# Kernel optimization log

Measured on AMD Instinct MI355X. Metric: run time of the kernel, lower is better.

## Reference

```python
import jax, jax.numpy as jnp
import numpy as np

D_MODEL = 2048
NUM_HEADS = 16
HEAD_DIM = D_MODEL // NUM_HEADS
B, S = 2, 2048


def setup_inputs() -> dict:
    key = jax.random.key(0)
    ks = jax.random.split(key, 11)
    scale = 1.0 / np.sqrt(D_MODEL)
    inp = {
        "query": jax.random.normal(ks[0], (B, S, D_MODEL), dtype=jnp.float32),
        "key": jax.random.normal(ks[1], (B, S, D_MODEL), dtype=jnp.float32),
        "value": jax.random.normal(ks[2], (B, S, D_MODEL), dtype=jnp.float32),
        "Wq": jax.random.normal(ks[3], (D_MODEL, D_MODEL), dtype=jnp.float32) * scale,
        "bq": jax.random.normal(ks[4], (D_MODEL,), dtype=jnp.float32) * 0.01,
        "Wk": jax.random.normal(ks[5], (D_MODEL, D_MODEL), dtype=jnp.float32) * scale,
        "bk": jax.random.normal(ks[6], (D_MODEL,), dtype=jnp.float32) * 0.01,
        "Wv": jax.random.normal(ks[7], (D_MODEL, D_MODEL), dtype=jnp.float32) * scale,
        "bv": jax.random.normal(ks[8], (D_MODEL,), dtype=jnp.float32) * 0.01,
        "Wo": jax.random.normal(ks[9], (D_MODEL, D_MODEL), dtype=jnp.float32) * scale,
        "bo": jax.random.normal(ks[10], (D_MODEL,), dtype=jnp.float32) * 0.01,
    }
    return inp


def _shape(x, B, S):
    # [B, S, D] -> [B, H, S, hd]
    return x.reshape(B, S, NUM_HEADS, HEAD_DIM).transpose(0, 2, 1, 3)


def reference(query, key, value, Wq, bq, Wk, bk, Wv, bv, Wo, bo):
    B, Sq, D = query.shape
    Sk = key.shape[1]
    # Linear layers (torch: y = x @ W.T + b)
    Q = _shape(query @ Wq.T + bq, B, Sq)   # [B,H,Sq,hd]
    K = _shape(key @ Wk.T + bk, B, Sk)     # [B,H,Sk,hd]
    V = _shape(value @ Wv.T + bv, B, Sk)   # [B,H,Sk,hd]
    scores = jnp.einsum('bhqd,bhkd->bhqk', Q, K) / jnp.sqrt(jnp.float32(HEAD_DIM))
    # causal mask: triu(ones(Sq, Sk), diagonal=1)
    causal = jnp.triu(jnp.ones((Sq, Sk), dtype=bool), k=1)
    scores = jnp.where(causal[None, None, :, :], jnp.float32(-jnp.inf), scores)
    attn = jax.nn.softmax(scores, axis=-1)
    out = jnp.einsum('bhqk,bhkd->bhqd', attn, V)
    out = out.transpose(0, 2, 1, 3).reshape(B, Sq, D)
    return out @ Wo.T + bo
```

## Files before the change

### kernel.cpp

```cpp
#include <hip/hip_runtime.h>
#include <hip/hip_bf16.h>

typedef __attribute__((ext_vector_type(8))) short short8;
typedef __attribute__((ext_vector_type(4))) short s16x4;
typedef __attribute__((ext_vector_type(4))) float f32x4;

#define MFMA_BF16(A, B, C) __builtin_amdgcn_mfma_f32_16x16x32_bf16(A, B, C, 0, 0, 0)

__device__ __forceinline__ void gload_lds16(const __hip_bfloat16* g, __hip_bfloat16* l) {
  __builtin_amdgcn_global_load_lds(
      (const __attribute__((address_space(1))) unsigned int*)g,
      (__attribute__((address_space(3))) unsigned int*)l, 16, 0, 0);
}

__device__ __forceinline__ float finite_or(float x, float repl) {
  unsigned u;
  __builtin_memcpy(&u, &x, 4);
  return ((u & 0x7f800000u) == 0x7f800000u) ? repl : x;
}

__device__ __forceinline__ short bf16_bits(float x) {
  __hip_bfloat16 b = __float2bfloat16(x);
  short s;
  __builtin_memcpy(&s, &b, 2);
  return s;
}

__device__ __forceinline__ short8 pack8(f32x4 a, f32x4 b) {
  short8 r;
  r[0] = bf16_bits(a[0]); r[1] = bf16_bits(a[1]);
  r[2] = bf16_bits(a[2]); r[3] = bf16_bits(a[3]);
  r[4] = bf16_bits(b[0]); r[5] = bf16_bits(b[1]);
  r[6] = bf16_bits(b[2]); r[7] = bf16_bits(b[3]);
  return r;
}

__global__ __launch_bounds__(256) void cvt_kernel(
    const float* x0, const float* x1, const float* x2,
    const float* w0, const float* w1, const float* w2, const float* w3,
    __hip_bfloat16* y0, __hip_bfloat16* y1, __hip_bfloat16* y2,
    __hip_bfloat16* u0, __hip_bfloat16* u1, __hip_bfloat16* u2, __hip_bfloat16* u3)
{
  const int z = blockIdx.y;
  const float* s = z == 0 ? x0 : z == 1 ? x1 : z == 2 ? x2
                 : z == 3 ? w0 : z == 4 ? w1 : z == 5 ? w2 : w3;
  __hip_bfloat16* d = z == 0 ? y0 : z == 1 ? y1 : z == 2 ? y2
                    : z == 3 ? u0 : z == 4 ? u1 : z == 5 ? u2 : u3;
  const size_t n = (z < 3) ? (size_t)8388608 : (size_t)4194304;
  const size_t stride = (size_t)gridDim.x * 256 * 8;
  for (size_t i = ((size_t)blockIdx.x * 256 + threadIdx.x) * 8; i < n; i += stride) {
    f32x4 a = *(const f32x4*)(s + i);
    f32x4 b = *(const f32x4*)(s + i + 4);
    *(short8*)((short*)d + i) = pack8(a, b);
  }
}

#define GBUF 24576

__device__ __forceinline__ void stage_A(const __hip_bfloat16* Ab, __hip_bfloat16* bufA,
                                        int kcol, int t, int wave) {
#pragma unroll
  for (int r = 0; r < 2; ++r) {
    const int ci = r * 512 + t;
    const int row = ci >> 3, c = ci & 7;
    const int sc = c ^ (row & 7);
    gload_lds16(Ab + (size_t)row * 2048 + kcol + sc * 8, bufA + r * 4096 + wave * 512);
  }
}
__device__ __forceinline__ void stage_Br(const __hip_bfloat16* Bb, __hip_bfloat16* bufB,
                                         int kcol, int t, int wave, int r) {
  const int ci = r * 512 + t;
  const int row = ci >> 3, c = ci & 7;
  const int sc = c ^ (row & 7);
  gload_lds16(Bb + (size_t)row * 2048 + kcol + sc * 8, bufB + r * 4096 + wave * 512);
}

template <typename OutT, bool BIAS_ROW>
__device__ __forceinline__ void gemm8p_body(
    const __hip_bfloat16* __restrict__ A, const __hip_bfloat16* __restrict__ Bt,
    const float* __restrict__ bias, OutT* __restrict__ C,
    int m0, int n0, int N, float trip, __hip_bfloat16* sm)
{
  constexpr int K = 2048, NT = K / 64;
  const int t = threadIdx.x, wave = t >> 6, lane = t & 63;
  const int ll = lane & 15, lg = lane >> 4;
  const int wmB = (wave >> 2) * 64, wnB = (wave & 3) * 64;
  const __hip_bfloat16* Ab = A + (size_t)m0 * K;
  const __hip_bfloat16* Bb = Bt + (size_t)n0 * K;

  f32x4 acc[4][4] = {};

  stage_A(Ab, sm, 0, t, wave);
  stage_Br(Bb, sm + 8192, 0, t, wave, 0);
  stage_Br(Bb, sm + 8192, 0, t, wave, 1);
  stage_Br(Bb, sm + 8192, 0, t, wave, 2);
  stage_Br(Bb, sm + 8192, 0, t, wave, 3);
  stage_A(Ab, sm + GBUF, 64, t, wave);
  stage_Br(Bb, sm + GBUF + 8192, 64, t, wave, 0);
  stage_Br(Bb, sm + GBUF + 8192, 64, t, wave, 1);
  stage_Br(Bb, sm + GBUF + 8192, 64, t, wave, 2);
  stage_Br(Bb, sm + GBUF + 8192, 64, t, wave, 3);
  asm volatile("s_waitcnt vmcnt(6)" ::: "memory");
  __builtin_amdgcn_s_barrier();

  for (int i = 0; i < NT; ++i) {
    const __hip_bfloat16* bufA = sm + (i % 3) * GBUF;
    const __hip_bfloat16* bufB = bufA + 8192;
    const bool pf = (i + 2 < NT);
    __hip_bfloat16* pA = sm + ((i + 2) % 3) * GBUF;
    const int pk = (i + 2) * 64;

#pragma unroll
    for (int kk = 0; kk < 2; ++kk) {
      short8 af[4], bf[4];
#pragma unroll
      for (int f = 0; f < 4; ++f) {
        const int ar = wmB + f * 16 + ll;
        af[f] = *(const short8*)&bufA[ar * 64 + (((kk * 4 + lg) ^ (ar & 7)) << 3)];
        const int br = wnB + f * 16 + ll;
        bf[f] = *(const short8*)&bufB[br * 64 + (((kk * 4 + lg) ^ (br & 7)) << 3)];
      }
      if (pf) {
        if (kk == 0) {
          stage_A(Ab, pA, pk, t, wave);
          stage_Br(Bb, pA + 8192, pk, t, wave, 0);
        } else {
          stage_Br(Bb, pA + 8192, pk, t, wave, 1);
          stage_Br(Bb, pA + 8192, pk, t, wave, 2);
          stage_Br(Bb, pA + 8192, pk, t, wave, 3);
        }
      }
      asm volatile("s_waitcnt lgkmcnt(0)" ::: "memory");
      __builtin_amdgcn_sched_barrier(0);
      __builtin_amdgcn_s_setprio(1);
#pragma unroll
      for (int mi = 0; mi < 4; ++mi)
#pragma unroll
        for (int ni = 0; ni < 4; ++ni)
          acc[mi][ni] = MFMA_BF16(af[mi], bf[ni], acc[mi][ni]);
      __builtin_amdgcn_s_setprio(0);
      __builtin_amdgcn_sched_barrier(0);
    }

    const int rem = NT - 1 - i;
    if (rem >= 2) {
      asm volatile("s_waitcnt vmcnt(6)" ::: "memory");
      __builtin_amdgcn_s_barrier();
    } else if (rem == 1) {
      asm volatile("s_waitcnt vmcnt(0)" ::: "memory");
      __builtin_amdgcn_s_barrier();
    }
  }

#pragma unroll
  for (int mi = 0; mi < 4; ++mi)
#pragma unroll
    for (int ni = 0; ni < 4; ++ni) {
      const int col = n0 + wnB + ni * 16 + ll;
      const float bcol = BIAS_ROW ? 0.f : bias[col];
#pragma unroll
      for (int j = 0; j < 4; ++j) {
        const int row = m0 + wmB + mi * 16 + lg * 4 + j;
        const float bv = BIAS_ROW ? bias[row] : bcol;
        const float val = finite_or(acc[mi][ni][j] + bv, trip);
        if constexpr (__is_same(OutT, float))
          C[(size_t)row * N + col] = val;
        else
          C[(size_t)row * N + col] = __float2bfloat16(val);
      }
    }
}

__global__ __launch_bounds__(512) void gemm_qkvvt_kernel(
    const __hip_bfloat16* xq, const __hip_bfloat16* xk, const __hip_bfloat16* xv,
    const __hip_bfloat16* Wq, const __hip_bfloat16* Wk, const __hip_bfloat16* Wv,
    const float* bq, const float* bk, const float* bv,
    __hip_bfloat16* Q, __hip_bfloat16* K, __hip_bfloat16* Vt2)
{
  __shared__ __align__(16) __hip_bfloat16 sm[3 * GBUF];
  const int L = (int)blockIdx.x;
  if (L < 512) {
    const int z = L & 1;
    const int r = L >> 1;
    const int n0 = (r & 7) * 256;
    const int m0 = (r >> 3) * 128;
    gemm8p_body<__hip_bfloat16, false>(z ? xk : xq, z ? Wk : Wq, z ? bk : bq,
                                       z ? K : Q, m0, n0, 2048, 20000.0f, sm);
  } else {
    const int r = L - 512;
    const int n0 = (r & 15) * 256;
    const int m0 = (r >> 4) * 128;
    gemm8p_body<__hip_bfloat16, true>(Wv, xv, bv, Vt2, m0, n0, 4096, 30000.0f, sm);
  }
}

__global__ __launch_bounds__(512) void gemm_out_kernel(
    const __hip_bfloat16* A, const __hip_bfloat16* W, const float* b, float* C)
{
  __shared__ __align__(16) __hip_bfloat16 sm[3 * GBUF];
  gemm8p_body<float, false>(A, W, b, C, (int)blockIdx.y * 128,
                            (int)blockIdx.x * 256, 2048, 50000.0f, sm);
}

__global__ __launch_bounds__(256) void attn_kernel(
    const __hip_bfloat16* __restrict__ Qb, const __hip_bfloat16* __restrict__ Kb,
    const __hip_bfloat16* __restrict__ Vt, __hip_bfloat16* __restrict__ Ob)
{
  constexpr int S = 2048, D = 2048, HD = 128;
  __shared__ __align__(16) __hip_bfloat16 Ks[2][64 * 128];
  __shared__ __align__(16) __hip_bfloat16 Vs[2][128 * 64];
  __shared__ __align__(16) short Ps[4][16 * 64];

  const int t = threadIdx.x, wave = t >> 6, lane = t & 63;
  const int lg = lane >> 4, ll = lane & 15;
  const int L = (int)blockIdx.x;
  const int bh = ((L & 7) << 2) | ((L >> 3) & 3);
  const int px = L >> 5;
  const int b = bh >> 4, h = bh & 15;
  char* const Psw = (char*)&Ps[wave][0];

  auto stageKV = [&](int buf, int kv0) {
#pragma unroll
    for (int r = 0; r < 4; ++r) {
      const int s = r * 256 + t;
      const int row = s >> 4, ch = s & 15;
      const int sc = ch ^ (row & 7);
      gload_lds16(Kb + (size_t)(b * S + kv0 + row) * D + h * HD + sc * 8,
                  &Ks[buf][0] + r * 2048 + wave * 512);
    }
#pragma unroll
    for (int r = 0; r < 4; ++r) {
      const int s = r * 256 + t;
      const int d = s >> 3, ch = s & 7;
      const int sc = ch ^ (d & 7);
      gload_lds16(Vt + (size_t)(h * HD + d) * (2 * S) + b * S + kv0 + sc * 8,
                  &Vs[buf][0] + r * 2048 + wave * 512);
    }
  };

  for (int ph = 0; ph < 2; ++ph) {
    const int qi = (ph == 0) ? px : 31 - px;
    const int q0 = qi * 64;
    const int qrow = q0 + wave * 16 + ll;

    short8 qf[4];
    const __hip_bfloat16* qptr = Qb + (size_t)(b * S + qrow) * D + h * HD + lg * 8;
#pragma unroll
    for (int kc = 0; kc < 4; ++kc) qf[kc] = *(const short8*)(qptr + kc * 32);

    f32x4 oacc[8] = {};
    float mrun = -1e30f, lrun = 0.f;

    __builtin_amdgcn_s_barrier();
    stageKV(0, 0);

    for (int tk = 0; tk <= qi; ++tk) {
      const int cur = tk & 1, nxt = cur ^ 1;
      __builtin_amdgcn_s_barrier();
      const bool pf = (tk < qi);
      if (pf) stageKV(nxt, (tk + 1) * 64);
      if (pf) asm volatile("s_waitcnt vmcnt(8)" ::: "memory");
      else    asm volatile("s_waitcnt vmcnt(0)" ::: "memory");
      __builtin_amdgcn_s_barrier();

      const int kv0 = tk * 64;
      const __hip_bfloat16* Kc = &Ks[cur][0];
      const __hip_bfloat16* Vc = &Vs[cur][0];

      f32x4 sacc[4] = {};
#pragma unroll
      for (int nf = 0; nf < 4; ++nf) {
        const int krow = nf * 16 + ll;
#pragma unroll
        for (int kc = 0; kc < 4; ++kc) {
          const int sw = (kc * 4 + lg) ^ (krow & 7);
          const short8 kf = *(const short8*)&Kc[krow * 128 + sw * 8];
          sacc[nf] = MFMA_BF16(kf, qf[kc], sacc[nf]);
        }
      }

      float sv[4][4];
      float mx = -1e30f;
#pragma unroll
      for (int nf = 0; nf < 4; ++nf)
#pragma unroll
        for (int j = 0; j < 4; ++j) {
          float s = sacc[nf][j] * 0.08838834764831845f;
          if (kv0 + nf * 16 + lg * 4 + j > qrow) s = -1e30f;
          sv[nf][j] = s;
          mx = fmaxf(mx, s);
        }
      mx = fmaxf(mx, __shfl_xor(mx, 16));
      mx = fmaxf(mx, __shfl_xor(mx, 32));
      const float mnew = fmaxf(mrun, mx);
      const float alpha = __expf(mrun - mnew);
      mrun = mnew;

      float rs = 0.f;
#pragma unroll
      for (int nf = 0; nf < 4; ++nf) {
        s16x4 pk;
#pragma unroll
        for (int j = 0; j < 4; ++j) {
          const float p = __expf(sv[nf][j] - mnew);
          rs += p;
          pk[j] = bf16_bits(p);
        }
        const int chunk = (nf * 2 + (lg >> 1)) ^ (ll & 7);
        *(s16x4*)(Psw + ll * 128 + chunk * 16 + (lg & 1) * 8) = pk;
      }
      rs += __shfl_xor(rs, 16);
      rs += __shfl_xor(rs, 32);
      lrun = lrun * alpha + rs;
#pragma unroll
      for (int df = 0; df < 8; ++df)
#pragma unroll
        for (int j = 0; j < 4; ++j) oacc[df][j] *= alpha;

      asm volatile("s_waitcnt lgkmcnt(0)" ::: "memory");
      __builtin_amdgcn_sched_barrier(0);

#pragma unroll
      for (int ks = 0; ks < 2; ++ks) {
        const int pchunk = (ks * 4 + lg) ^ (ll & 7);
        const short8 pf8 = *(const short8*)(Psw + ll * 128 + pchunk * 16);
#pragma unroll
        for (int df = 0; df < 8; ++df) {
          const int vrow = df * 16 + ll;
          const int sw = (ks * 4 + lg) ^ (vrow & 7);
          const short8 vf = *(const short8*)&Vc[vrow * 64 + sw * 8];
          oacc[df] = MFMA_BF16(vf, pf8, oacc[df]);
        }
      }
    }

    const float inv = 1.0f / lrun;
#pragma unroll
    for (int df = 0; df < 8; ++df) {
      s16x4 o;
#pragma unroll
      for (int j = 0; j < 4; ++j)
        o[j] = bf16_bits(finite_or(oacc[df][j] * inv, 300.0f));
      *(s16x4*)(Ob + (size_t)(b * S + qrow) * D + h * HD + df * 16 + lg * 4) = o;
    }
  }
}

extern "C" void kernel_launch(void* const* d_in, const int* in_sizes, int n_in,
                              void* d_out, int out_size, void* d_ws, size_t ws_size,
                              hipStream_t stream)
{
  const float* q  = (const float*)d_in[0];
  const float* k  = (const float*)d_in[1];
  const float* v  = (const float*)d_in[2];
  const float* Wq = (const float*)d_in[3];
  const float* bq = (const float*)d_in[4];
  const float* Wk = (const float*)d_in[5];
  const float* bk = (const float*)d_in[6];
  const float* Wv = (const float*)d_in[7];
  const float* bv = (const float*)d_in[8];
  const float* Wo = (const float*)d_in[9];
  const float* bo = (const float*)d_in[10];

  char* wsb = (char*)d_ws;
  const size_t MB = 1024 * 1024;
  __hip_bfloat16* Qw  = (__hip_bfloat16*)(wsb + 0 * MB);
  __hip_bfloat16* Kw  = (__hip_bfloat16*)(wsb + 16 * MB);
  __hip_bfloat16* Vt2 = (__hip_bfloat16*)(wsb + 32 * MB);
  __hip_bfloat16* xqb = (__hip_bfloat16*)(wsb + 48 * MB);
  __hip_bfloat16* xkb = (__hip_bfloat16*)(wsb + 64 * MB);
  __hip_bfloat16* xvb = (__hip_bfloat16*)(wsb + 80 * MB);
  __hip_bfloat16* Wqb = (__hip_bfloat16*)(wsb + 96 * MB);
  __hip_bfloat16* Wkb = (__hip_bfloat16*)(wsb + 104 * MB);
  __hip_bfloat16* Wvb = (__hip_bfloat16*)(wsb + 112 * MB);
  __hip_bfloat16* Wob = (__hip_bfloat16*)(wsb + 120 * MB);
  __hip_bfloat16* Ow  = xkb;

  cvt_kernel<<<dim3(1024, 7), 256, 0, stream>>>(
      q, k, v, Wq, Wk, Wv, Wo, xqb, xkb, xvb, Wqb, Wkb, Wvb, Wob);
  gemm_qkvvt_kernel<<<dim3(768), 512, 0, stream>>>(
      xqb, xkb, xvb, Wqb, Wkb, Wvb, bq, bk, bv, Qw, Kw, Vt2);
  attn_kernel<<<dim3(512), 256, 0, stream>>>(Qw, Kw, Vt2, Ow);
  gemm_out_kernel<<<dim3(8, 32), 512, 0, stream>>>(
      Ow, Wob, bo, (float*)d_out);
}
```

Baseline: 270.2 us.

## Split attention into one block per query tile and drop KV double buffering

The attention kernel previously ran 512 blocks, each processing a paired light and heavy causal query tile in two phases with double-buffered K/V staging. Now 1024 blocks each handle a single query tile, ordered so that consecutive blocks interleave light and heavy tiles, and K/V use a single LDS buffer loaded synchronously each iteration. Halving LDS use and doubling the block count aims for higher occupancy and more parallelism, with other resident blocks hiding load latency. The cost is that prefetch overlap inside each block is lost, since every KV tile load waits on vmcnt(0) before any compute starts.

Result: no change. 269.4 us, median of 2 (-0.3%).

```diff
diff --git a/kernel.cpp b/kernel.cpp
--- a/kernel.cpp
+++ b/kernel.cpp
@@ -207,26 +207,31 @@
     const __hip_bfloat16* __restrict__ Vt, __hip_bfloat16* __restrict__ Ob)
 {
   constexpr int S = 2048, D = 2048, HD = 128;
-  __shared__ __align__(16) __hip_bfloat16 Ks[2][64 * 128];
-  __shared__ __align__(16) __hip_bfloat16 Vs[2][128 * 64];
+  __shared__ __align__(16) __hip_bfloat16 Ks[64 * 128];
+  __shared__ __align__(16) __hip_bfloat16 Vs[128 * 64];
   __shared__ __align__(16) short Ps[4][16 * 64];
 
   const int t = threadIdx.x, wave = t >> 6, lane = t & 63;
   const int lg = lane >> 4, ll = lane & 15;
   const int L = (int)blockIdx.x;
   const int bh = ((L & 7) << 2) | ((L >> 3) & 3);
-  const int px = L >> 5;
+  const int p = L >> 5;
+  const int a = p & 7, bq_ = p >> 3;
+  const int qi = (bq_ == 0) ? a : (bq_ == 1) ? 15 - a
+               : (bq_ == 2) ? 16 + a : 31 - a;
   const int b = bh >> 4, h = bh & 15;
+  const int q0 = qi * 64;
+  const int qrow = q0 + wave * 16 + ll;
   char* const Psw = (char*)&Ps[wave][0];
 
-  auto stageKV = [&](int buf, int kv0) {
+  auto stageKV = [&](int kv0) {
 #pragma unroll
     for (int r = 0; r < 4; ++r) {
       const int s = r * 256 + t;
       const int row = s >> 4, ch = s & 15;
       const int sc = ch ^ (row & 7);
       gload_lds16(Kb + (size_t)(b * S + kv0 + row) * D + h * HD + sc * 8,
-                  &Ks[buf][0] + r * 2048 + wave * 512);
+                  Ks + r * 2048 + wave * 512);
     }
 #pragma unroll
     for (int r = 0; r < 4; ++r) {
@@ -234,115 +239,100 @@
       const int d = s >> 3, ch = s & 7;
       const int sc = ch ^ (d & 7);
       gload_lds16(Vt + (size_t)(h * HD + d) * (2 * S) + b * S + kv0 + sc * 8,
-                  &Vs[buf][0] + r * 2048 + wave * 512);
+                  Vs + r * 2048 + wave * 512);
     }
   };
 
-  for (int ph = 0; ph < 2; ++ph) {
-    const int qi = (ph == 0) ? px : 31 - px;
-    const int q0 = qi * 64;
-    const int qrow = q0 + wave * 16 + ll;
-
-    short8 qf[4];
-    const __hip_bfloat16* qptr = Qb + (size_t)(b * S + qrow) * D + h * HD + lg * 8;
-#pragma unroll
-    for (int kc = 0; kc < 4; ++kc) qf[kc] = *(const short8*)(qptr + kc * 32);
-
-    f32x4 oacc[8] = {};
-    float mrun = -1e30f, lrun = 0.f;
-
+  short8 qf[4];
+  const __hip_bfloat16* qptr = Qb + (size_t)(b * S + qrow) * D + h * HD + lg * 8;
+#pragma unroll
+  for (int kc = 0; kc < 4; ++kc) qf[kc] = *(const short8*)(qptr + kc * 32);
+
+  f32x4 oacc[8] = {};
+  float mrun = -1e30f, lrun = 0.f;
+
+  for (int tk = 0; tk <= qi; ++tk) {
+    const int kv0 = tk * 64;
     __builtin_amdgcn_s_barrier();
-    stageKV(0, 0);
-
-    for (int tk = 0; tk <= qi; ++tk) {
-      const int cur = tk & 1, nxt = cur ^ 1;
-      __builtin_amdgcn_s_barrier();
-      const bool pf = (tk < qi);
-      if (pf) stageKV(nxt, (tk + 1) * 64);
-      if (pf) asm volatile("s_waitcnt vmcnt(8)" ::: "memory");
-      else    asm volatile("s_waitcnt vmcnt(0)" ::: "memory");
-      __builtin_amdgcn_s_barrier();
-
-      const int kv0 = tk * 64;
-      const __hip_bfloat16* Kc = &Ks[cur][0];
-      const __hip_bfloat16* Vc = &Vs[cur][0];
-
-      f32x4 sacc[4] = {};
-#pragma unroll
-      for (int nf = 0; nf < 4; ++nf) {
-        const int krow = nf * 16 + ll;
-#pragma unroll
-        for (int kc = 0; kc < 4; ++kc) {
-          const int sw = (kc * 4 + lg) ^ (krow & 7);
-          const short8 kf = *(const short8*)&Kc[krow * 128 + sw * 8];
-          sacc[nf] = MFMA_BF16(kf, qf[kc], sacc[nf]);
-        }
-      }
-
-      float sv[4][4];
-      float mx = -1e30f;
-#pragma unroll
-      for (int nf = 0; nf < 4; ++nf)
-#pragma unroll
-        for (int j = 0; j < 4; ++j) {
-          float s = sacc[nf][j] * 0.08838834764831845f;
-          if (kv0 + nf * 16 + lg * 4 + j > qrow) s = -1e30f;
-          sv[nf][j] = s;
-          mx = fmaxf(mx, s);
-        }
-      mx = fmaxf(mx, __shfl_xor(mx, 16));
-      mx = fmaxf(mx, __shfl_xor(mx, 32));
-      const float mnew = fmaxf(mrun, mx);
-      const float alpha = __expf(mrun - mnew);
-      mrun = mnew;
-
-      float rs = 0.f;
-#pragma unroll
-      for (int nf = 0; nf < 4; ++nf) {
-        s16x4 pk;
-#pragma unroll
-        for (int j = 0; j < 4; ++j) {
-          const float p = __expf(sv[nf][j] - mnew);
-          rs += p;
-          pk[j] = bf16_bits(p);
-        }
-        const int chunk = (nf * 2 + (lg >> 1)) ^ (ll & 7);
-        *(s16x4*)(Psw + ll * 128 + chunk * 16 + (lg & 1) * 8) = pk;
-      }
-      rs += __shfl_xor(rs, 16);
-      rs += __shfl_xor(rs, 32);
-      lrun = lrun * alpha + rs;
-#pragma unroll
-      for (int df = 0; df < 8; ++df)
-#pragma unroll
-        for (int j = 0; j < 4; ++j) oacc[df][j] *= alpha;
-
-      asm volatile("s_waitcnt lgkmcnt(0)" ::: "memory");
-      __builtin_amdgcn_sched_barrier(0);
-
-#pragma unroll
-      for (int ks = 0; ks < 2; ++ks) {
-        const int pchunk = (ks * 4 + lg) ^ (ll & 7);
-        const short8 pf8 = *(const short8*)(Psw + ll * 128 + pchunk * 16);
-#pragma unroll
-        for (int df = 0; df < 8; ++df) {
-          const int vrow = df * 16 + ll;
-          const int sw = (ks * 4 + lg) ^ (vrow & 7);
-          const short8 vf = *(const short8*)&Vc[vrow * 64 + sw * 8];
-          oacc[df] = MFMA_BF16(vf, pf8, oacc[df]);
-        }
-      }
-    }
-
-    const float inv = 1.0f / lrun;
-#pragma unroll
-    for (int df = 0; df < 8; ++df) {
-      s16x4 o;
-#pragma unroll
-      for (int j = 0; j < 4; ++j)
-        o[j] = bf16_bits(finite_or(oacc[df][j] * inv, 300.0f));
-      *(s16x4*)(Ob + (size_t)(b * S + qrow) * D + h * HD + df * 16 + lg * 4) = o;
-    }
+    stageKV(kv0);
+    asm volatile("s_waitcnt vmcnt(0)" ::: "memory");
+    __builtin_amdgcn_s_barrier();
+
+    f32x4 sacc[4] = {};
+#pragma unroll
+    for (int nf = 0; nf < 4; ++nf) {
+      const int krow = nf * 16 + ll;
+#pragma unroll
+      for (int kc = 0; kc < 4; ++kc) {
+        const int sw = (kc * 4 + lg) ^ (krow & 7);
+        const short8 kf = *(const short8*)&Ks[krow * 128 + sw * 8];
+        sacc[nf] = MFMA_BF16(kf, qf[kc], sacc[nf]);
+      }
+    }
+
+    float sv[4][4];
+    float mx = -1e30f;
+#pragma unroll
+    for (int nf = 0; nf < 4; ++nf)
+#pragma unroll
+      for (int j = 0; j < 4; ++j) {
+        float s = sacc[nf][j] * 0.08838834764831845f;
+        if (kv0 + nf * 16 + lg * 4 + j > qrow) s = -1e30f;
+        sv[nf][j] = s;
+        mx = fmaxf(mx, s);
+      }
+    mx = fmaxf(mx, __shfl_xor(mx, 16));
+    mx = fmaxf(mx, __shfl_xor(mx, 32));
+    const float mnew = fmaxf(mrun, mx);
+    const float alpha = __expf(mrun - mnew);
+    mrun = mnew;
+
+    float rs = 0.f;
+#pragma unroll
+    for (int nf = 0; nf < 4; ++nf) {
+      s16x4 pk;
+#pragma unroll
+      for (int j = 0; j < 4; ++j) {
+        const float pv = __expf(sv[nf][j] - mnew);
+        rs += pv;
+        pk[j] = bf16_bits(pv);
+      }
+      const int chunk = (nf * 2 + (lg >> 1)) ^ (ll & 7);
+      *(s16x4*)(Psw + ll * 128 + chunk * 16 + (lg & 1) * 8) = pk;
+    }
+    rs += __shfl_xor(rs, 16);
+    rs += __shfl_xor(rs, 32);
+    lrun = lrun * alpha + rs;
+#pragma unroll
+    for (int df = 0; df < 8; ++df)
+#pragma unroll
+      for (int j = 0; j < 4; ++j) oacc[df][j] *= alpha;
+
+    asm volatile("s_waitcnt lgkmcnt(0)" ::: "memory");
+    __builtin_amdgcn_sched_barrier(0);
+
+#pragma unroll
+    for (int ks = 0; ks < 2; ++ks) {
+      const int pchunk = (ks * 4 + lg) ^ (ll & 7);
+      const short8 pf8 = *(const short8*)(Psw + ll * 128 + pchunk * 16);
+#pragma unroll
+      for (int df = 0; df < 8; ++df) {
+        const int vrow = df * 16 + ll;
+        const int sw = (ks * 4 + lg) ^ (vrow & 7);
+        const short8 vf = *(const short8*)&Vs[vrow * 64 + sw * 8];
+        oacc[df] = MFMA_BF16(vf, pf8, oacc[df]);
+      }
+    }
+  }
+
+  const float inv = 1.0f / lrun;
+#pragma unroll
+  for (int df = 0; df < 8; ++df) {
+    s16x4 o;
+#pragma unroll
+    for (int j = 0; j < 4; ++j)
+      o[j] = bf16_bits(finite_or(oacc[df][j] * inv, 300.0f));
+    *(s16x4*)(Ob + (size_t)(b * S + qrow) * D + h * HD + df * 16 + lg * 4) = o;
   }
 }
 
@@ -380,7 +370,7 @@
       q, k, v, Wq, Wk, Wv, Wo, xqb, xkb, xvb, Wqb, Wkb, Wvb, Wob);
   gemm_qkvvt_kernel<<<dim3(768), 512, 0, stream>>>(
       xqb, xkb, xvb, Wqb, Wkb, Wvb, bq, bk, bv, Qw, Kw, Vt2);
-  attn_kernel<<<dim3(512), 256, 0, stream>>>(Qw, Kw, Vt2, Ow);
+  attn_kernel<<<dim3(1024), 256, 0, stream>>>(Qw, Kw, Vt2, Ow);
   gemm_out_kernel<<<dim3(8, 32), 512, 0, stream>>>(
       Ow, Wob, bo, (float*)d_out);
 }
```
